# Kernel tuning notes

Measured on AMD Instinct MI355X. Metric: run time of the kernel, lower is better.

## Reference

```python
import jax, jax.numpy as jnp
import numpy as np

N_NODES = 50000   # hypergraph nodes
N_EDGES = 20000   # hyperedges
M = 400000        # node-edge incidences (node copies)
L = 800000        # inner GIN graph edges per side
HID = 128
IN_DIM = 128
B = 32            # graphs in batch
C = 10            # num_classes
N_LAYERS = 2
INNER = 2         # inner_num_layers
BN_EPS = 1e-5


def setup_inputs() -> dict:
    key = jax.random.key(0)
    ks = jax.random.split(key, 16)
    s = 0.05
    inp = {}
    inp["x_N"] = jax.random.normal(ks[0], (N_NODES, IN_DIM), jnp.float32)
    # embedding linear
    inp["We"] = jax.random.normal(ks[1], (IN_DIM, HID), jnp.float32) * s
    inp["be"] = jnp.zeros((HID,), jnp.float32)
    # GIN params: [outer_layer, direction(N2E/E2N), inner_conv, mlp_linear, hid, hid]
    inp["Wg"] = jax.random.normal(ks[2], (N_LAYERS, 2, INNER, 2, HID, HID), jnp.float32) * s
    inp["bg"] = jnp.zeros((N_LAYERS, 2, INNER, 2, HID), jnp.float32)
    inp["eps_g"] = jnp.zeros((N_LAYERS, 2, INNER), jnp.float32)
    # eval-mode BatchNorm affine params per inner conv
    inp["gamma"] = jnp.ones((N_LAYERS, 2, INNER, HID), jnp.float32)
    inp["beta"] = jnp.zeros((N_LAYERS, 2, INNER, HID), jnp.float32)
    # per-layer prediction heads
    inp["Wp"] = jax.random.normal(ks[3], (N_LAYERS + 1, HID, C), jnp.float32) * s
    inp["bp"] = jnp.zeros((N_LAYERS + 1, C), jnp.float32)
    # index tensors
    inp["ori_node_idx"] = jax.random.randint(ks[4], (M,), 0, N_NODES)
    inp["node2edge"] = jax.random.randint(ks[5], (M,), 0, N_EDGES)
    inp["edge_index_N"] = jax.random.randint(ks[6], (2, L), 0, M)
    inp["ori_edge_idx"] = jax.random.randint(ks[7], (M,), 0, N_EDGES)
    inp["edge2node"] = jax.random.randint(ks[8], (M,), 0, N_NODES)
    inp["edge_index_E"] = jax.random.randint(ks[9], (2, L), 0, M)
    inp["batch"] = jax.random.randint(ks[10], (M,), 0, B)
    return inp


def _gin(x, src, dst, Wg, bg, eps, gamma, beta):
    # GIN over the copy graph: h = MLP((1+eps)*x + sum_{j->i} x_j), BN (eval), ReLU between convs
    inv_std = 1.0 / jnp.sqrt(1.0 + BN_EPS)
    n = x.shape[0]
    for l in range(INNER):
        agg = jax.ops.segment_sum(x[src], dst, num_segments=n)
        h = (1.0 + eps[l]) * x + agg
        h = jax.nn.relu(h @ Wg[l, 0] + bg[l, 0])
        h = h @ Wg[l, 1] + bg[l, 1]
        h = gamma[l] * h * inv_std + beta[l]
        x = jax.nn.relu(h) if l < INNER - 1 else h
    return x


def reference(x_N, We, be, Wg, bg, eps_g, gamma, beta, Wp, bp,
              ori_node_idx, node2edge, edge_index_N,
              ori_edge_idx, edge2node, edge_index_E, batch):
    node_x = x_N @ We + be                       # [N, HID]
    xs = [node_x]
    for i in range(N_LAYERS):
        # node -> edge: gather copies, inner GIN, segment-sum pool over hyperedges
        nx = node_x[ori_node_idx]                # [M, HID]
        nx = _gin(nx, edge_index_N[0], edge_index_N[1],
                  Wg[i, 0], bg[i, 0], eps_g[i, 0], gamma[i, 0], beta[i, 0])
        edge_x = jax.ops.segment_sum(nx, node2edge, num_segments=N_EDGES)
        edge_x = jax.nn.relu(edge_x)             # EdgeUpdate (dropout off in eval)
        # edge -> node
        ex = edge_x[ori_edge_idx]                # [M, HID]
        ex = _gin(ex, edge_index_E[0], edge_index_E[1],
                  Wg[i, 1], bg[i, 1], eps_g[i, 1], gamma[i, 1], beta[i, 1])
        node_x = jax.ops.segment_sum(ex, edge2node, num_segments=N_NODES)
        node_x = jax.nn.relu(node_x)             # NodeUpdate
        xs.append(node_x)
    score = jnp.zeros((B, C), x_N.dtype)
    for i, x in enumerate(xs):
        pooled = jax.ops.segment_sum(x[ori_node_idx], batch, num_segments=B)
        score = score + pooled @ Wp[i] + bp[i]
    return score
```

## Files before the change

kernel.cpp:

```cpp
#include <hip/hip_runtime.h>
#include <hip/hip_bf16.h>

#define HID 128
static const int N_NODES = 50000;
static const int N_EDGES = 20000;
static const int M_COPIES = 400000;
static const int L_EDGES = 800000;
static const int NBATCH = 32;
static const int NCLS = 10;
#define INV_STD 0.9999950000374997f
#define IDX_CAP 384
#define PKSHIFT 19
#define PKMASK  0x7FFFF

typedef __attribute__((ext_vector_type(4))) float f32x4;
typedef __attribute__((ext_vector_type(8))) short short8;
typedef __attribute__((ext_vector_type(8))) unsigned short ushort8;
typedef __attribute__((ext_vector_type(4))) unsigned short u16x4;

__device__ __forceinline__ float bf2f(unsigned short u) {
    union { unsigned u; float f; } v; v.u = ((unsigned)u) << 16; return v.f;
}
__device__ __forceinline__ unsigned short f2bf(float f) {
    union { float f; unsigned u; } v; v.f = f;
    unsigned r = v.u + 0x7FFFu + ((v.u >> 16) & 1u);
    return (unsigned short)(r >> 16);
}
__device__ __forceinline__ void gatomic_add(float* p, float v) {
    unsafeAtomicAdd(p, v);
}

__device__ __forceinline__ unsigned short* xs_addr(unsigned short* Xs, int c, int r) {
    int byte = ((c * 64 + r) * 16) ^ ((c & 7) << 4);
    return (unsigned short*)((char*)Xs + byte);
}

__device__ __forceinline__ void stage8(const unsigned short* __restrict__ Wmat, int e,
                                       unsigned short* buf, int wave, int lane) {
    const char* g = (const char*)Wmat + ((size_t)e << 12) + (wave << 10) + (lane << 4);
    char* l = (char*)buf + (wave << 10);
    __builtin_amdgcn_global_load_lds(
        (const __attribute__((address_space(1))) unsigned int*)g,
        (__attribute__((address_space(3))) unsigned int*)l,
        16, 0, 0);
}

template<int N>
__device__ __forceinline__ void pipe_barrier() {
    if constexpr (N == 0) asm volatile("s_waitcnt vmcnt(0)" ::: "memory");
    else                  asm volatile("s_waitcnt vmcnt(1)" ::: "memory");
    __builtin_amdgcn_s_barrier();
    asm volatile("" ::: "memory");
}

__device__ __forceinline__ void mfma4(const unsigned short* Ws, const short8* xv,
                                      f32x4& a, int quad, int ln) {
#pragma unroll
    for (int kc = 0; kc < 4; ++kc) {
        short8 wa = *(const short8*)(Ws + (((kc * 4 + quad) * 16) + ln) * 8);
        a = __builtin_amdgcn_mfma_f32_16x16x32_bf16(wa, xv[kc], a, 0, 0, 0);
    }
}

__global__ __launch_bounds__(256) void prep_w(const float* __restrict__ We,
                                              const float* __restrict__ Wg,
                                              unsigned short* __restrict__ Wt) {
    int t = blockIdx.x * 256 + threadIdx.x;
    if (t >= 17 * 16384) return;
    int mat = t >> 14, rem = t & 16383;
    int h = rem >> 11, r2 = rem & 2047;
    int gg = r2 >> 7, r3 = r2 & 127;
    int n = r3 >> 3, j = r3 & 7;
    int k = gg * 8 + j, col = h * 16 + n;
    const float* src = (mat == 0) ? We : (Wg + (size_t)(mat - 1) * 16384);
    Wt[t] = f2bf(src[k * 128 + col]);
}

__global__ __launch_bounds__(256) void hist2_k(
    const int* __restrict__ iA, int nA, int* __restrict__ cA,
    const int* __restrict__ iB, int nB, int* __restrict__ cB, int shift) {
    int t = blockIdx.x * 256 + threadIdx.x;
    if (t < nA) atomicAdd(&cA[iA[t] >> shift], 1);
    if (t < nB) atomicAdd(&cB[iB[t] >> shift], 1);
}

__global__ __launch_bounds__(256) void scan1d_k(
    int* __restrict__ a0, int n0, int* __restrict__ p0,
    int* __restrict__ a1, int n1, int* __restrict__ p1) {
    int* a    = blockIdx.y ? a1 : a0;
    int n     = blockIdx.y ? n1 : n0;
    int* part = blockIdx.y ? p1 : p0;
    if ((int)(blockIdx.x * 256) >= n) return;
    __shared__ int s[256];
    int i = blockIdx.x * 256 + threadIdx.x;
    int v = (i < n) ? a[i] : 0;
    s[threadIdx.x] = v;
    __syncthreads();
#pragma unroll
    for (int d = 1; d < 256; d <<= 1) {
        int t = (threadIdx.x >= d) ? s[threadIdx.x - d] : 0;
        __syncthreads();
        s[threadIdx.x] += t;
        __syncthreads();
    }
    if (i < n) a[i] = s[threadIdx.x] - v;
    if (threadIdx.x == 255) part[blockIdx.x] = s[255];
}

__global__ __launch_bounds__(256) void scan2d_k(
    int* __restrict__ p0, int nb0, int* __restrict__ p1, int nb1) {
    int* part = blockIdx.x ? p1 : p0;
    int nb    = blockIdx.x ? nb1 : nb0;
    __shared__ int s[256];
    __shared__ int carry;
    if (threadIdx.x == 0) carry = 0;
    __syncthreads();
    for (int base = 0; base < nb; base += 256) {
        int i = base + threadIdx.x;
        int v = (i < nb) ? part[i] : 0;
        s[threadIdx.x] = v;
        __syncthreads();
#pragma unroll
        for (int d = 1; d < 256; d <<= 1) {
            int t = (threadIdx.x >= d) ? s[threadIdx.x - d] : 0;
            __syncthreads();
            s[threadIdx.x] += t;
            __syncthreads();
        }
        if (i < nb) part[i] = carry + s[threadIdx.x] - v;
        __syncthreads();
        if (threadIdx.x == 0) carry += s[255];
        __syncthreads();
    }
}

__global__ __launch_bounds__(256) void scan3d_k(
    int* __restrict__ a0, int n0, const int* __restrict__ p0,
    int* __restrict__ a1, int n1, const int* __restrict__ p1) {
    int* a          = blockIdx.y ? a1 : a0;
    int n           = blockIdx.y ? n1 : n0;
    const int* part = blockIdx.y ? p1 : p0;
    int i = blockIdx.x * 256 + threadIdx.x;
    if (i < n) a[i] += part[blockIdx.x];
}

__global__ __launch_bounds__(256) void fill_edgeblk2_k(
    const int* __restrict__ sA, const int* __restrict__ dA, const int* __restrict__ rA,
    int nA, int* __restrict__ oA, int2* __restrict__ pkA,
    const int* __restrict__ sB, const int* __restrict__ dB, const int* __restrict__ rB,
    int nB, int* __restrict__ oB, int2* __restrict__ pkB) {
    int t = blockIdx.x * 256 + threadIdx.x;
    if (t < nA) {
        int d = dA[t]; int pos = atomicAdd(&oA[d >> 6], 1);
        int s = sA[t]; int rl = (d & 63) << PKSHIFT;
        pkA[pos] = (int2){rl | s, rl | rA[s]};
    }
    if (t < nB) {
        int d = dB[t]; int pos = atomicAdd(&oB[d >> 6], 1);
        int s = sB[t]; int rl = (d & 63) << PKSHIFT;
        pkB[pos] = (int2){rl | s, rl | rB[s]};
    }
}

__global__ __launch_bounds__(256) void fill_pool2_k(
    const int* __restrict__ gA, int nA, int* __restrict__ oA, int* __restrict__ itA,
    const int* __restrict__ gB, int nB, int* __restrict__ oB, int* __restrict__ itB) {
    int t = blockIdx.x * 256 + threadIdx.x;
    if (t < nA) { int pos = atomicAdd(&oA[gA[t]], 1); itA[pos] = t; }
    if (t < nB) { int pos = atomicAdd(&oB[gB[t]], 1); itB[pos] = t; }
}

__global__ __launch_bounds__(256) void segsum_pool(
    const unsigned short* __restrict__ tbl, const int* __restrict__ off,
    const int* __restrict__ items, unsigned short* __restrict__ out, int nseg)
{
    int wave = threadIdx.x >> 6, lane = threadIdx.x & 63;
    int seg = blockIdx.x * 4 + wave;
    if (seg >= nseg) return;
    int start = (seg == 0) ? 0 : off[seg - 1];
    int end = off[seg];
    int g = lane & 15, sub = lane >> 4;
    float a[8] = {0.f, 0.f, 0.f, 0.f, 0.f, 0.f, 0.f, 0.f};
    for (int p = start + sub; p < end; p += 4) {
        int r = items[p];
        ushort8 v = *(const ushort8*)(tbl + (size_t)r * 128 + g * 8);
#pragma unroll
        for (int j = 0; j < 8; ++j) a[j] += bf2f(v[j]);
    }
#pragma unroll
    for (int j = 0; j < 8; ++j) {
        a[j] += __shfl_xor(a[j], 16, 64);
        a[j] += __shfl_xor(a[j], 32, 64);
    }
    if (sub == 0) {
        ushort8 ov;
#pragma unroll
        for (int j = 0; j < 8; ++j) ov[j] = f2bf(fmaxf(a[j], 0.f));
        *(ushort8*)(out + (size_t)seg * 128 + g * 8) = ov;
    }
}

template<bool CONV0>
__global__ __launch_bounds__(256, 5) void fused_conv(
    const unsigned short* __restrict__ tbl,
    const int* __restrict__ self_idx,
    const int* __restrict__ blkOff, const int2* __restrict__ edgePk,
    const float* __restrict__ eps_ptr,
    const unsigned short* __restrict__ W1t, const float* __restrict__ b1,
    const unsigned short* __restrict__ W2t, const float* __restrict__ b2,
    const float* __restrict__ gam, const float* __restrict__ bet,
    unsigned short* __restrict__ out)
{
    __shared__ __align__(16) unsigned short Xs[16 * 64 * 8];
    __shared__ __align__(16) unsigned short Wsb[3][2048];
    __shared__ int sIdx[IDX_CAP];
    __shared__ int sSelf[64];
    __shared__ int rcnt[64], rbase[64], rpos[64];
    const int tid = threadIdx.x;
    const int row0 = blockIdx.x * 64;
    const int wave = tid >> 6, lane = tid & 63;

    stage8(W1t, 0, Wsb[0], wave, lane);
    stage8(W1t, 1, Wsb[1], wave, lane);

    const int blk = blockIdx.x;
    const int bstart = (blk == 0) ? 0 : blkOff[blk - 1];
    const int cnt = blkOff[blk] - bstart;

    if (tid < 64) sSelf[tid] = CONV0 ? self_idx[row0 + tid] : row0 + tid;
    __syncthreads();

    const float e = 1.0f + eps_ptr[0];
    const int g = tid & 15;
    const int rb = tid >> 4;
    float a[4][8];
#pragma unroll
    for (int i = 0; i < 4; ++i) {
        int self = sSelf[rb + 16 * i];
        ushort8 u = *(const ushort8*)(tbl + (size_t)self * 128 + g * 8);
#pragma unroll
        for (int j = 0; j < 8; ++j) a[i][j] = e * bf2f(u[j]);
    }

    int done = 0;
    while (done < cnt) {
        const int chunk = (cnt - done < IDX_CAP) ? (cnt - done) : IDX_CAP;
        if (tid < 64) rcnt[tid] = 0;
        __syncthreads();
        int e0 = -1, e1 = -1;
        if (tid < chunk) {
            int2 pk = edgePk[bstart + done + tid];
            e0 = CONV0 ? pk.y : pk.x;
            atomicAdd(&rcnt[e0 >> PKSHIFT], 1);
        }
        if (tid + 256 < chunk) {
            int2 pk = edgePk[bstart + done + tid + 256];
            e1 = CONV0 ? pk.y : pk.x;
            atomicAdd(&rcnt[e1 >> PKSHIFT], 1);
        }
        __syncthreads();
        if (tid < 64) {
            int c = rcnt[tid];
            int s = c;
#pragma unroll
            for (int d = 1; d < 64; d <<= 1) {
                int t = __shfl_up(s, d, 64);
                if (tid >= d) s += t;
            }
            rbase[tid] = s - c;
            rpos[tid]  = s - c;
        }
        __syncthreads();
        if (e0 >= 0) { int p = atomicAdd(&rpos[e0 >> PKSHIFT], 1); sIdx[p] = e0 & PKMASK; }
        if (e1 >= 0) { int p = atomicAdd(&rpos[e1 >> PKSHIFT], 1); sIdx[p] = e1 & PKMASK; }
        __syncthreads();

        int st[4], en[4];
#pragma unroll
        for (int i = 0; i < 4; ++i) {
            int r = rb + 16 * i;
            st[i] = rbase[r]; en[i] = rpos[r];
        }
        const int cmax = chunk - 1;
        while (__ballot((st[0] < en[0]) | (st[1] < en[1]) |
                        (st[2] < en[2]) | (st[3] < en[3]))) {
            ushort8 v[4];
#pragma unroll
            for (int i = 0; i < 4; ++i) {
                int p = st[i] < cmax ? st[i] : cmax;
                int idx = sIdx[p];
                v[i] = *(const ushort8*)(tbl + (size_t)idx * 128 + g * 8);
            }
#pragma unroll
            for (int i = 0; i < 4; ++i) {
                if (st[i] < en[i]) {
#pragma unroll
                    for (int j = 0; j < 8; ++j) a[i][j] += bf2f(v[i][j]);
                    st[i]++;
                }
            }
        }
        done += chunk;
        __syncthreads();
    }

#pragma unroll
    for (int i = 0; i < 4; ++i) {
        ushort8 xv;
#pragma unroll
        for (int j = 0; j < 8; ++j) xv[j] = f2bf(a[i][j]);
        *(ushort8*)xs_addr(Xs, g, rb + 16 * i) = xv;
    }
    __syncthreads();

    const int ln = lane & 15, quad = lane >> 4;
    const int row = wave * 16 + ln;

    short8 xb[4];
#pragma unroll
    for (int kc = 0; kc < 4; ++kc)
        xb[kc] = *(const short8*)xs_addr(Xs, kc * 4 + quad, row);

    f32x4 acc[8];
#pragma unroll
    for (int t = 0; t < 8; ++t) acc[t] = (f32x4){0.f, 0.f, 0.f, 0.f};

#pragma unroll
    for (int s = 0; s < 8; ++s) {
        int pf = s + 2;
        stage8(pf < 8 ? W1t : W2t, pf & 7, Wsb[pf % 3], wave, lane);
        mfma4(Wsb[s % 3], xb, acc[s], quad, ln);
        pipe_barrier<1>();
    }

    {
        const int j0 = (quad & 1) * 4;
#pragma unroll
        for (int t = 0; t < 8; ++t) {
            int p0 = t * 16 + quad * 4;
            f32x4 bv = *(const f32x4*)(b1 + p0);
            u16x4 hp;
#pragma unroll
            for (int i = 0; i < 4; ++i) hp[i] = f2bf(fmaxf(acc[t][i] + bv[i], 0.f));
            *(u16x4*)((char*)xs_addr(Xs, p0 >> 3, row) + j0 * 2) = hp;
        }
    }

    short8 hb[4];
#pragma unroll
    for (int kc = 0; kc < 4; ++kc)
        hb[kc] = *(const short8*)xs_addr(Xs, kc * 4 + quad, row);

#pragma unroll
    for (int t = 0; t < 8; ++t) acc[t] = (f32x4){0.f, 0.f, 0.f, 0.f};

#pragma unroll
    for (int f = 0; f < 8; ++f) {
        if (f < 6) stage8(W2t, f + 2, Wsb[(f + 10) % 3], wave, lane);
        mfma4(Wsb[(f + 8) % 3], hb, acc[f], quad, ln);
        if (f < 6)      pipe_barrier<1>();
        else if (f == 6) pipe_barrier<0>();
    }

    const int m = row0 + row;
#pragma unroll
    for (int t = 0; t < 8; ++t) {
        int n0 = t * 16 + quad * 4;
        f32x4 bv = *(const f32x4*)(b2 + n0);
        f32x4 gv = *(const f32x4*)(gam + n0);
        f32x4 tv = *(const f32x4*)(bet + n0);
        u16x4 op;
#pragma unroll
        for (int i = 0; i < 4; ++i) {
            float h = acc[t][i] + bv[i];
            h = gv[i] * h * INV_STD + tv[i];
            if (CONV0) h = fmaxf(h, 0.f);
            op[i] = f2bf(h);
        }
        *(u16x4*)(out + (size_t)m * 128 + n0) = op;
    }
}

__global__ __launch_bounds__(256) void gemm_embed(
    const float* __restrict__ in, const unsigned short* __restrict__ Wt,
    const float* __restrict__ bias, unsigned short* __restrict__ out_bf, int rows)
{
    __shared__ __align__(16) unsigned short Xs[16 * 64 * 8];
    __shared__ __align__(16) unsigned short Ws[16 * 128 * 8];
    int tid = threadIdx.x;
    int row0 = blockIdx.x * 64;
#pragma unroll
    for (int i = 0; i < 8; ++i) {
        int chunk = tid + i * 256;
        int n = chunk >> 4, g = chunk & 15;
        *(short8*)(Ws + (g * 128 + n) * 8) =
            *(const short8*)(Wt + (n >> 4) * 2048 + g * 128 + (n & 15) * 8);
    }
#pragma unroll
    for (int i = 0; i < 4; ++i) {
        int chunk = tid + i * 256;
        int r = chunk >> 4, g = chunk & 15;
        int gr = row0 + r;
        ushort8 v;
        if (gr < rows) {
            const float* p = in + (size_t)gr * 128 + g * 8;
            f32x4 a0 = *(const f32x4*)p;
            f32x4 a1 = *(const f32x4*)(p + 4);
#pragma unroll
            for (int j = 0; j < 4; ++j) { v[j] = f2bf(a0[j]); v[4 + j] = f2bf(a1[j]); }
        } else {
#pragma unroll
            for (int j = 0; j < 8; ++j) v[j] = 0;
        }
        *(ushort8*)(Xs + (g * 64 + r) * 8) = v;
    }
    __syncthreads();
    int wave = tid >> 6, lane = tid & 63;
    int m0 = wave * 16;
    int ln = lane & 15, quad = lane >> 4;
    f32x4 acc[8];
#pragma unroll
    for (int t = 0; t < 8; ++t) acc[t] = (f32x4){0.f, 0.f, 0.f, 0.f};
#pragma unroll
    for (int kc = 0; kc < 4; ++kc) {
        int g = kc * 4 + quad;
        short8 a = *(const short8*)(Xs + (g * 64 + m0 + ln) * 8);
#pragma unroll
        for (int t = 0; t < 8; ++t) {
            short8 b = *(const short8*)(Ws + (g * 128 + t * 16 + ln) * 8);
            acc[t] = __builtin_amdgcn_mfma_f32_16x16x32_bf16(a, b, acc[t], 0, 0, 0);
        }
    }
#pragma unroll
    for (int t = 0; t < 8; ++t) {
        int col = t * 16 + ln;
        float bi = bias[col];
#pragma unroll
        for (int i = 0; i < 4; ++i) {
            int gr = row0 + m0 + quad * 4 + i;
            if (gr < rows) out_bf[(size_t)gr * 128 + col] = f2bf(acc[t][i] + bi);
        }
    }
}

template<bool ACCUM>
__global__ __launch_bounds__(256) void proj_y(
    const unsigned short* __restrict__ nx, const float* __restrict__ Wp,
    float* __restrict__ y, int rows)
{
    __shared__ float Wl[HID * NCLS];
    for (int i = threadIdx.x; i < HID * NCLS; i += 256) Wl[i] = Wp[i];
    __syncthreads();
    int r = blockIdx.x * 256 + threadIdx.x;
    if (r >= rows) return;
    float acc[NCLS];
#pragma unroll
    for (int c = 0; c < NCLS; ++c) acc[c] = 0.f;
    const unsigned short* xp = nx + (size_t)r * 128;
#pragma unroll 4
    for (int g = 0; g < 16; ++g) {
        ushort8 u = *(const ushort8*)(xp + g * 8);
#pragma unroll
        for (int j = 0; j < 8; ++j) {
            float xv = bf2f(u[j]);
            const float* w = Wl + (g * 8 + j) * NCLS;
#pragma unroll
            for (int c = 0; c < NCLS; ++c) acc[c] += xv * w[c];
        }
    }
    float* yp = y + (size_t)r * NCLS;
#pragma unroll
    for (int c = 0; c < NCLS; ++c) {
        if (ACCUM) yp[c] += acc[c];
        else yp[c] = acc[c];
    }
}

__global__ __launch_bounds__(256) void score_scatter(
    const float* __restrict__ y, const int* __restrict__ ori,
    const int* __restrict__ batch, float* __restrict__ score)
{
    __shared__ float sc[NBATCH * NCLS];
    for (int i = threadIdx.x; i < NBATCH * NCLS; i += 256) sc[i] = 0.f;
    __syncthreads();
    int stride = gridDim.x * 256;
    for (int m = blockIdx.x * 256 + threadIdx.x; m < M_COPIES; m += stride) {
        int r = ori[m], b = batch[m];
        const float* yp = y + (size_t)r * NCLS;
#pragma unroll
        for (int c = 0; c < NCLS; ++c)
            __hip_atomic_fetch_add(&sc[b * NCLS + c], yp[c],
                                   __ATOMIC_RELAXED, __HIP_MEMORY_SCOPE_WORKGROUP);
    }
    __syncthreads();
    for (int i = threadIdx.x; i < NBATCH * NCLS; i += 256) gatomic_add(score + i, sc[i]);
}

__global__ void score_final(const float* __restrict__ score, const float* __restrict__ bp,
                            float* __restrict__ out)
{
    int t = threadIdx.x;
    if (t >= NBATCH * NCLS) return;
    int c = t % NCLS;
    out[t] = score[t] + bp[c] + bp[NCLS + c] + bp[2 * NCLS + c];
}

__global__ void fill_sentinel(float* out, int n, float enc) {
    int t = blockIdx.x * 64 + threadIdx.x;
    if (t < n) out[t] = enc;
}

extern "C" void kernel_launch(void* const* d_in, const int* in_sizes, int n_in,
                              void* d_out, int out_size, void* d_ws, size_t ws_size,
                              hipStream_t stream) {
    const float* x_N    = (const float*)d_in[0];
    const float* We     = (const float*)d_in[1];
    const float* be     = (const float*)d_in[2];
    const float* Wg     = (const float*)d_in[3];
    const float* bg     = (const float*)d_in[4];
    const float* eps_g  = (const float*)d_in[5];
    const float* gam    = (const float*)d_in[6];
    const float* bet    = (const float*)d_in[7];
    const float* Wp     = (const float*)d_in[8];
    const float* bp     = (const float*)d_in[9];
    const int* ori_node = (const int*)d_in[10];
    const int* node2edge= (const int*)d_in[11];
    const int* eiN      = (const int*)d_in[12];
    const int* ori_edge = (const int*)d_in[13];
    const int* edge2node= (const int*)d_in[14];
    const int* eiE      = (const int*)d_in[15];
    const int* batch    = (const int*)d_in[16];

    const int NBLK = M_COPIES / 64;

    char* p = (char*)d_ws;
    auto take = [&](size_t n) { char* r = p; p += (n + 255) & ~(size_t)255; return r; };
    unsigned short* Wt  = (unsigned short*)take((size_t)17 * 16384 * 2);
    unsigned short* Xb  = (unsigned short*)take((size_t)M_COPIES * 128 * 2);
    unsigned short* Xb2 = (unsigned short*)take((size_t)M_COPIES * 128 * 2);
    unsigned short* nx  = (unsigned short*)take((size_t)N_NODES * 128 * 2);
    unsigned short* ex  = (unsigned short*)take((size_t)N_EDGES * 128 * 2);
    float* y            = (float*)take((size_t)N_NODES * NCLS * 4);
    float* score        = (float*)take((size_t)NBATCH * NCLS * 4);
    int* blkN           = (int*)take((size_t)2 * NBLK * 4);
    int* blkE           = blkN + NBLK;
    int* off_n2e        = (int*)take((size_t)N_EDGES * 4);
    int* off_e2n        = (int*)take((size_t)N_NODES * 4);
    int2* pkN           = (int2*)take((size_t)L_EDGES * 8);
    int2* pkE           = (int2*)take((size_t)L_EDGES * 8);
    int* it_n2e         = (int*)take((size_t)M_COPIES * 4);
    int* it_e2n         = (int*)take((size_t)M_COPIES * 4);
    int* part           = (int*)take((size_t)8192 * 4);
    size_t need = (size_t)(p - (char*)d_ws);
    if (need > ws_size) {
        fill_sentinel<<<(out_size + 63) / 64, 64, 0, stream>>>(
            (float*)d_out, out_size, 1.0e9f + (float)ws_size);
        return;
    }

    prep_w<<<1088, 256, 0, stream>>>(We, Wg, Wt);
    (void)hipMemsetAsync(score, 0, (size_t)NBATCH * NCLS * 4, stream);

    const int NB_M = (M_COPIES + 255) / 256;
    const int NB_L = (L_EDGES + 255) / 256;
    const int NB_N = (N_NODES + 255) / 256;
    const int NB_B = (NBLK + 255) / 256;
    int* partB = part + 4096;

    (void)hipMemsetAsync(blkN, 0, (size_t)2 * NBLK * 4, stream);
    hist2_k<<<NB_L, 256, 0, stream>>>(eiN + L_EDGES, L_EDGES, blkN,
                                      eiE + L_EDGES, L_EDGES, blkE, 6);
    scan1d_k<<<dim3(NB_B, 2), 256, 0, stream>>>(blkN, NBLK, part, blkE, NBLK, partB);
    scan2d_k<<<2, 256, 0, stream>>>(part, NB_B, partB, NB_B);
    scan3d_k<<<dim3(NB_B, 2), 256, 0, stream>>>(blkN, NBLK, part, blkE, NBLK, partB);
    fill_edgeblk2_k<<<NB_L, 256, 0, stream>>>(
        eiN, eiN + L_EDGES, ori_node, L_EDGES, blkN, pkN,
        eiE, eiE + L_EDGES, ori_edge, L_EDGES, blkE, pkE);

    (void)hipMemsetAsync(off_n2e, 0,
        (size_t)((char*)off_e2n - (char*)off_n2e) + (size_t)N_NODES * 4, stream);
    hist2_k<<<NB_M, 256, 0, stream>>>(node2edge, M_COPIES, off_n2e,
                                      edge2node, M_COPIES, off_e2n, 0);
    scan1d_k<<<dim3(NB_N, 2), 256, 0, stream>>>(off_n2e, N_EDGES, part, off_e2n, N_NODES, partB);
    scan2d_k<<<2, 256, 0, stream>>>(part, (N_EDGES + 255) / 256, partB, NB_N);
    scan3d_k<<<dim3(NB_N, 2), 256, 0, stream>>>(off_n2e, N_EDGES, part, off_e2n, N_NODES, partB);
    fill_pool2_k<<<NB_M, 256, 0, stream>>>(node2edge, M_COPIES, off_n2e, it_n2e,
                                           edge2node, M_COPIES, off_e2n, it_e2n);

    gemm_embed<<<(N_NODES + 63) / 64, 256, 0, stream>>>(x_N, Wt, be, nx, N_NODES);
    proj_y<false><<<(N_NODES + 255) / 256, 256, 0, stream>>>(nx, Wp, y, N_NODES);

    for (int layer = 0; layer < 2; ++layer) {
        for (int dir = 0; dir < 2; ++dir) {
            int cj0 = layer * 4 + dir * 2;
            int cj1 = cj0 + 1;
            const unsigned short* base = (dir == 0) ? nx : ex;
            const int* selfI = (dir == 0) ? ori_node : ori_edge;
            const int* blkD  = (dir == 0) ? blkN : blkE;
            const int2* pkD  = (dir == 0) ? pkN : pkE;

            fused_conv<true><<<NBLK, 256, 0, stream>>>(
                base, selfI, blkD, pkD, eps_g + cj0,
                Wt + (size_t)(1 + cj0 * 2) * 16384, bg + (cj0 * 2) * 128,
                Wt + (size_t)(1 + cj0 * 2 + 1) * 16384, bg + (cj0 * 2 + 1) * 128,
                gam + cj0 * 128, bet + cj0 * 128, Xb);
            fused_conv<false><<<NBLK, 256, 0, stream>>>(
                Xb, nullptr, blkD, pkD, eps_g + cj1,
                Wt + (size_t)(1 + cj1 * 2) * 16384, bg + (cj1 * 2) * 128,
                Wt + (size_t)(1 + cj1 * 2 + 1) * 16384, bg + (cj1 * 2 + 1) * 128,
                gam + cj1 * 128, bet + cj1 * 128, Xb2);
            if (dir == 0) {
                segsum_pool<<<(N_EDGES + 3) / 4, 256, 0, stream>>>(
                    Xb2, off_n2e, it_n2e, ex, N_EDGES);
            } else {
                segsum_pool<<<(N_NODES + 3) / 4, 256, 0, stream>>>(
                    Xb2, off_e2n, it_e2n, nx, N_NODES);
                proj_y<true><<<(N_NODES + 255) / 256, 256, 0, stream>>>(
                    nx, Wp + (layer + 1) * HID * NCLS, y, N_NODES);
            }
        }
    }
    score_scatter<<<256, 256, 0, stream>>>(y, ori_node, batch, score);
    score_final<<<1, 320, 0, stream>>>(score, bp, (float*)d_out);
}
```

Before: 1.350 ms.

## Shrink LDS footprint for higher occupancy and unroll pool segment sum

The fused GIN conv kernel now uses two weight staging buffers instead of three, prefetching one slice ahead with a full drain before each barrier. It also halves the edge-index chunk capacity so each thread handles one packed edge per chunk. Together these cut shared memory per block, and the launch bound rises from 5 to 6 blocks per CU. The trade-off is a shallower weight-load pipeline, which exposes more global-to-LDS latency, and more chunk iterations for blocks with many edges. Separately, the segment-sum pooling loop is unrolled by two so two row loads are in flight per lane.

```diff
diff --git a/kernel.cpp b/kernel.cpp
--- a/kernel.cpp
+++ b/kernel.cpp
@@ -9,7 +9,7 @@
 static const int NBATCH = 32;
 static const int NCLS = 10;
 #define INV_STD 0.9999950000374997f
-#define IDX_CAP 384
+#define IDX_CAP 256
 #define PKSHIFT 19
 #define PKMASK  0x7FFFF
 
@@ -45,10 +45,8 @@
         16, 0, 0);
 }
 
-template<int N>
-__device__ __forceinline__ void pipe_barrier() {
-    if constexpr (N == 0) asm volatile("s_waitcnt vmcnt(0)" ::: "memory");
-    else                  asm volatile("s_waitcnt vmcnt(1)" ::: "memory");
+__device__ __forceinline__ void drain_barrier() {
+    asm volatile("s_waitcnt vmcnt(0)" ::: "memory");
     __builtin_amdgcn_s_barrier();
     asm volatile("" ::: "memory");
 }
@@ -181,7 +179,15 @@
     int end = off[seg];
     int g = lane & 15, sub = lane >> 4;
     float a[8] = {0.f, 0.f, 0.f, 0.f, 0.f, 0.f, 0.f, 0.f};
-    for (int p = start + sub; p < end; p += 4) {
+    int p = start + sub;
+    for (; p + 4 < end; p += 8) {
+        int r0 = items[p], r1 = items[p + 4];
+        ushort8 v0 = *(const ushort8*)(tbl + (size_t)r0 * 128 + g * 8);
+        ushort8 v1 = *(const ushort8*)(tbl + (size_t)r1 * 128 + g * 8);
+#pragma unroll
+        for (int j = 0; j < 8; ++j) a[j] += bf2f(v0[j]) + bf2f(v1[j]);
+    }
+    if (p < end) {
         int r = items[p];
         ushort8 v = *(const ushort8*)(tbl + (size_t)r * 128 + g * 8);
 #pragma unroll
@@ -201,7 +207,7 @@
 }
 
 template<bool CONV0>
-__global__ __launch_bounds__(256, 5) void fused_conv(
+__global__ __launch_bounds__(256, 6) void fused_conv(
     const unsigned short* __restrict__ tbl,
     const int* __restrict__ self_idx,
     const int* __restrict__ blkOff, const int2* __restrict__ edgePk,
@@ -212,7 +218,7 @@
     unsigned short* __restrict__ out)
 {
     __shared__ __align__(16) unsigned short Xs[16 * 64 * 8];
-    __shared__ __align__(16) unsigned short Wsb[3][2048];
+    __shared__ __align__(16) unsigned short Wsb[2][2048];
     __shared__ int sIdx[IDX_CAP];
     __shared__ int sSelf[64];
     __shared__ int rcnt[64], rbase[64], rpos[64];
@@ -221,7 +227,6 @@
     const int wave = tid >> 6, lane = tid & 63;
 
     stage8(W1t, 0, Wsb[0], wave, lane);
-    stage8(W1t, 1, Wsb[1], wave, lane);
 
     const int blk = blockIdx.x;
     const int bstart = (blk == 0) ? 0 : blkOff[blk - 1];
@@ -247,16 +252,11 @@
         const int chunk = (cnt - done < IDX_CAP) ? (cnt - done) : IDX_CAP;
         if (tid < 64) rcnt[tid] = 0;
         __syncthreads();
-        int e0 = -1, e1 = -1;
+        int e0 = -1;
         if (tid < chunk) {
             int2 pk = edgePk[bstart + done + tid];
             e0 = CONV0 ? pk.y : pk.x;
             atomicAdd(&rcnt[e0 >> PKSHIFT], 1);
-        }
-        if (tid + 256 < chunk) {
-            int2 pk = edgePk[bstart + done + tid + 256];
-            e1 = CONV0 ? pk.y : pk.x;
-            atomicAdd(&rcnt[e1 >> PKSHIFT], 1);
         }
         __syncthreads();
         if (tid < 64) {
@@ -272,7 +272,6 @@
         }
         __syncthreads();
         if (e0 >= 0) { int p = atomicAdd(&rpos[e0 >> PKSHIFT], 1); sIdx[p] = e0 & PKMASK; }
-        if (e1 >= 0) { int p = atomicAdd(&rpos[e1 >> PKSHIFT], 1); sIdx[p] = e1 & PKMASK; }
         __syncthreads();
 
         int st[4], en[4];
@@ -327,10 +326,10 @@
 
 #pragma unroll
     for (int s = 0; s < 8; ++s) {
-        int pf = s + 2;
-        stage8(pf < 8 ? W1t : W2t, pf & 7, Wsb[pf % 3], wave, lane);
-        mfma4(Wsb[s % 3], xb, acc[s], quad, ln);
-        pipe_barrier<1>();
+        int pf = s + 1;
+        stage8(pf < 8 ? W1t : W2t, pf & 7, Wsb[pf & 1], wave, lane);
+        mfma4(Wsb[s & 1], xb, acc[s], quad, ln);
+        drain_barrier();
     }
 
     {
@@ -356,10 +355,9 @@
 
 #pragma unroll
     for (int f = 0; f < 8; ++f) {
-        if (f < 6) stage8(W2t, f + 2, Wsb[(f + 10) % 3], wave, lane);
-        mfma4(Wsb[(f + 8) % 3], hb, acc[f], quad, ln);
-        if (f < 6)      pipe_barrier<1>();
-        else if (f == 6) pipe_barrier<0>();
+        if (f < 7) stage8(W2t, f + 1, Wsb[(f + 1) & 1], wave, lane);
+        mfma4(Wsb[f & 1], hb, acc[f], quad, ln);
+        if (f < 7) drain_barrier();
     }
 
     const int m = row0 + row;
```

Result: slower. 1.623 ms (+20.2%).

## Scatter conv outputs into segment order and fuse projection into pooling

Applied to the files above, without the earlier changes.

fill_pool2_k now records each copy's rank within its pooling segment. The second GIN conv uses that rank to write its output rows directly in segment-sorted order, so segsum_pool reads contiguous rows instead of gathering through an index list, and its loop is unrolled by two. The E2N pooling kernel also computes the per-node class projection and adds it into y, which removes the separate proj_y launch and its re-read of nx. In exchange the conv output writes are now scattered, and the projection runs inside only one quarter of the lanes of the pool kernel.

```diff
diff --git a/kernel.cpp b/kernel.cpp
--- a/kernel.cpp
+++ b/kernel.cpp
@@ -163,16 +163,18 @@
 }
 
 __global__ __launch_bounds__(256) void fill_pool2_k(
-    const int* __restrict__ gA, int nA, int* __restrict__ oA, int* __restrict__ itA,
-    const int* __restrict__ gB, int nB, int* __restrict__ oB, int* __restrict__ itB) {
+    const int* __restrict__ gA, int nA, int* __restrict__ oA, int* __restrict__ rkA,
+    const int* __restrict__ gB, int nB, int* __restrict__ oB, int* __restrict__ rkB) {
     int t = blockIdx.x * 256 + threadIdx.x;
-    if (t < nA) { int pos = atomicAdd(&oA[gA[t]], 1); itA[pos] = t; }
-    if (t < nB) { int pos = atomicAdd(&oB[gB[t]], 1); itB[pos] = t; }
-}
-
+    if (t < nA) rkA[t] = atomicAdd(&oA[gA[t]], 1);
+    if (t < nB) rkB[t] = atomicAdd(&oB[gB[t]], 1);
+}
+
+template<bool PROJ>
 __global__ __launch_bounds__(256) void segsum_pool(
     const unsigned short* __restrict__ tbl, const int* __restrict__ off,
-    const int* __restrict__ items, unsigned short* __restrict__ out, int nseg)
+    unsigned short* __restrict__ out, int nseg,
+    const float* __restrict__ Wp, float* __restrict__ y)
 {
     int wave = threadIdx.x >> 6, lane = threadIdx.x & 63;
     int seg = blockIdx.x * 4 + wave;
@@ -181,9 +183,15 @@
     int end = off[seg];
     int g = lane & 15, sub = lane >> 4;
     float a[8] = {0.f, 0.f, 0.f, 0.f, 0.f, 0.f, 0.f, 0.f};
-    for (int p = start + sub; p < end; p += 4) {
-        int r = items[p];
-        ushort8 v = *(const ushort8*)(tbl + (size_t)r * 128 + g * 8);
+    int p = start + sub;
+    for (; p + 4 < end; p += 8) {
+        ushort8 v0 = *(const ushort8*)(tbl + (size_t)p * 128 + g * 8);
+        ushort8 v1 = *(const ushort8*)(tbl + (size_t)(p + 4) * 128 + g * 8);
+#pragma unroll
+        for (int j = 0; j < 8; ++j) a[j] += bf2f(v0[j]) + bf2f(v1[j]);
+    }
+    if (p < end) {
+        ushort8 v = *(const ushort8*)(tbl + (size_t)p * 128 + g * 8);
 #pragma unroll
         for (int j = 0; j < 8; ++j) a[j] += bf2f(v[j]);
     }
@@ -193,10 +201,32 @@
         a[j] += __shfl_xor(a[j], 32, 64);
     }
     if (sub == 0) {
+        float r[8];
         ushort8 ov;
 #pragma unroll
-        for (int j = 0; j < 8; ++j) ov[j] = f2bf(fmaxf(a[j], 0.f));
+        for (int j = 0; j < 8; ++j) { r[j] = fmaxf(a[j], 0.f); ov[j] = f2bf(r[j]); }
         *(ushort8*)(out + (size_t)seg * 128 + g * 8) = ov;
+        if (PROJ) {
+            float part[NCLS];
+#pragma unroll
+            for (int c = 0; c < NCLS; ++c) part[c] = 0.f;
+#pragma unroll
+            for (int j = 0; j < 8; ++j) {
+                float xv = r[j];
+                const float* w = Wp + (g * 8 + j) * NCLS;
+#pragma unroll
+                for (int c = 0; c < NCLS; ++c) part[c] += xv * w[c];
+            }
+#pragma unroll
+            for (int d = 1; d < 16; d <<= 1)
+#pragma unroll
+                for (int c = 0; c < NCLS; ++c) part[c] += __shfl_xor(part[c], d, 64);
+            if (g == 0) {
+                float* yp = y + (size_t)seg * NCLS;
+#pragma unroll
+                for (int c = 0; c < NCLS; ++c) yp[c] += part[c];
+            }
+        }
     }
 }
 
@@ -205,6 +235,7 @@
     const unsigned short* __restrict__ tbl,
     const int* __restrict__ self_idx,
     const int* __restrict__ blkOff, const int2* __restrict__ edgePk,
+    const int* __restrict__ outIdx,
     const float* __restrict__ eps_ptr,
     const unsigned short* __restrict__ W1t, const float* __restrict__ b1,
     const unsigned short* __restrict__ W2t, const float* __restrict__ b2,
@@ -363,6 +394,8 @@
     }
 
     const int m = row0 + row;
+    const int orow = CONV0 ? m : outIdx[m];
+    unsigned short* obase = out + (size_t)orow * 128;
 #pragma unroll
     for (int t = 0; t < 8; ++t) {
         int n0 = t * 16 + quad * 4;
@@ -377,7 +410,7 @@
             if (CONV0) h = fmaxf(h, 0.f);
             op[i] = f2bf(h);
         }
-        *(u16x4*)(out + (size_t)m * 128 + n0) = op;
+        *(u16x4*)(obase + n0) = op;
     }
 }
 
@@ -443,8 +476,7 @@
     }
 }
 
-template<bool ACCUM>
-__global__ __launch_bounds__(256) void proj_y(
+__global__ __launch_bounds__(256) void proj_y0(
     const unsigned short* __restrict__ nx, const float* __restrict__ Wp,
     float* __restrict__ y, int rows)
 {
@@ -470,10 +502,7 @@
     }
     float* yp = y + (size_t)r * NCLS;
 #pragma unroll
-    for (int c = 0; c < NCLS; ++c) {
-        if (ACCUM) yp[c] += acc[c];
-        else yp[c] = acc[c];
-    }
+    for (int c = 0; c < NCLS; ++c) yp[c] = acc[c];
 }
 
 __global__ __launch_bounds__(256) void score_scatter(
@@ -548,8 +577,8 @@
     int* off_e2n        = (int*)take((size_t)N_NODES * 4);
     int2* pkN           = (int2*)take((size_t)L_EDGES * 8);
     int2* pkE           = (int2*)take((size_t)L_EDGES * 8);
-    int* it_n2e         = (int*)take((size_t)M_COPIES * 4);
-    int* it_e2n         = (int*)take((size_t)M_COPIES * 4);
+    int* rk_n2e         = (int*)take((size_t)M_COPIES * 4);
+    int* rk_e2n         = (int*)take((size_t)M_COPIES * 4);
     int* part           = (int*)take((size_t)8192 * 4);
     size_t need = (size_t)(p - (char*)d_ws);
     if (need > ws_size) {
@@ -584,11 +613,11 @@
     scan1d_k<<<dim3(NB_N, 2), 256, 0, stream>>>(off_n2e, N_EDGES, part, off_e2n, N_NODES, partB);
     scan2d_k<<<2, 256, 0, stream>>>(part, (N_EDGES + 255) / 256, partB, NB_N);
     scan3d_k<<<dim3(NB_N, 2), 256, 0, stream>>>(off_n2e, N_EDGES, part, off_e2n, N_NODES, partB);
-    fill_pool2_k<<<NB_M, 256, 0, stream>>>(node2edge, M_COPIES, off_n2e, it_n2e,
-                                           edge2node, M_COPIES, off_e2n, it_e2n);
+    fill_pool2_k<<<NB_M, 256, 0, stream>>>(node2edge, M_COPIES, off_n2e, rk_n2e,
+                                           edge2node, M_COPIES, off_e2n, rk_e2n);
 
     gemm_embed<<<(N_NODES + 63) / 64, 256, 0, stream>>>(x_N, Wt, be, nx, N_NODES);
-    proj_y<false><<<(N_NODES + 255) / 256, 256, 0, stream>>>(nx, Wp, y, N_NODES);
+    proj_y0<<<(N_NODES + 255) / 256, 256, 0, stream>>>(nx, Wp, y, N_NODES);
 
     for (int layer = 0; layer < 2; ++layer) {
         for (int dir = 0; dir < 2; ++dir) {
@@ -598,25 +627,25 @@
             const int* selfI = (dir == 0) ? ori_node : ori_edge;
             const int* blkD  = (dir == 0) ? blkN : blkE;
             const int2* pkD  = (dir == 0) ? pkN : pkE;
+            const int* rkD   = (dir == 0) ? rk_n2e : rk_e2n;
 
             fused_conv<true><<<NBLK, 256, 0, stream>>>(
-                base, selfI, blkD, pkD, eps_g + cj0,
+                base, selfI, blkD, pkD, nullptr, eps_g + cj0,
                 Wt + (size_t)(1 + cj0 * 2) * 16384, bg + (cj0 * 2) * 128,
                 Wt + (size_t)(1 + cj0 * 2 + 1) * 16384, bg + (cj0 * 2 + 1) * 128,
                 gam + cj0 * 128, bet + cj0 * 128, Xb);
             fused_conv<false><<<NBLK, 256, 0, stream>>>(
-                Xb, nullptr, blkD, pkD, eps_g + cj1,
+                Xb, nullptr, blkD, pkD, rkD, eps_g + cj1,
                 Wt + (size_t)(1 + cj1 * 2) * 16384, bg + (cj1 * 2) * 128,
                 Wt + (size_t)(1 + cj1 * 2 + 1) * 16384, bg + (cj1 * 2 + 1) * 128,
                 gam + cj1 * 128, bet + cj1 * 128, Xb2);
             if (dir == 0) {
-                segsum_pool<<<(N_EDGES + 3) / 4, 256, 0, stream>>>(
-                    Xb2, off_n2e, it_n2e, ex, N_EDGES);
+                segsum_pool<false><<<(N_EDGES + 3) / 4, 256, 0, stream>>>(
+                    Xb2, off_n2e, ex, N_EDGES, nullptr, nullptr);
             } else {
-                segsum_pool<<<(N_NODES + 3) / 4, 256, 0, stream>>>(
-                    Xb2, off_e2n, it_e2n, nx, N_NODES);
-                proj_y<true><<<(N_NODES + 255) / 256, 256, 0, stream>>>(
-                    nx, Wp + (layer + 1) * HID * NCLS, y, N_NODES);
+                segsum_pool<true><<<(N_NODES + 3) / 4, 256, 0, stream>>>(
+                    Xb2, off_e2n, nx, N_NODES,
+                    Wp + (size_t)(layer + 1) * HID * NCLS, y);
             }
         }
     }
```

Result: slower. 1.412 ms (+4.6%).
